# Optimization experiments

Measured on AMD Instinct MI355X. Metric: run time of the kernel, lower is better.

The kernel has to match this reference:

```python
import jax, jax.numpy as jnp
import numpy as np

N_NODES = 50000
N_EDGES = 300000
IN_DIM = 2000
DF = 128
H1, H2, OUT_DIM, K = 256, 128, 32, 4


def gcn_conv(x, W, b, src, dst, ew):
    """PyG GCNConv with edge weights: add self-loops (weight 1), symmetric norm."""
    N = x.shape[0]
    loop = jnp.arange(N)
    src2 = jnp.concatenate([src, loop])
    dst2 = jnp.concatenate([dst, loop])
    ew2 = jnp.concatenate([ew, jnp.ones((N,), ew.dtype)])
    deg = jax.ops.segment_sum(ew2, dst2, num_segments=N)
    dinv = jnp.where(deg > 0, jax.lax.rsqrt(deg), 0.0)
    norm = dinv[src2] * ew2 * dinv[dst2]            # [E+N]
    h = x @ W                                       # [N, out]
    out = jax.ops.segment_sum(norm[:, None] * h[src2], dst2, num_segments=N)
    return out + b


def setup_inputs() -> dict:
    key = jax.random.key(0)
    ks = jax.random.split(key, 13)
    p = lambda k, shape, s=0.05: (jax.random.normal(k, shape, jnp.float32) * s)
    return {
        "X": jax.random.normal(ks[0], (N_NODES, IN_DIM), jnp.float32),
        "edge_index": jax.random.randint(ks[1], (2, N_EDGES), 0, N_NODES),
        "Wh": p(ks[2], (IN_DIM, DF)),
        "mlp_W1": p(ks[3], (K, 2 * DF, 2)),
        "mlp_b1": jnp.zeros((K, 2), jnp.float32),
        "mlp_W2": p(ks[4], (K, 2, 1)),
        "mlp_b2": jnp.zeros((K, 1), jnp.float32),
        "g1_W": p(ks[5], (DF, H1)),
        "g1_b": jnp.zeros((H1,), jnp.float32),
        "g2_W": p(ks[6], (H1, H2)),
        "g2_b": jnp.zeros((H2,), jnp.float32),
        "fc_W": p(ks[7], (H2, OUT_DIM)),
        "fc_b": jnp.zeros((OUT_DIM,), jnp.float32),
    }


def reference(X, edge_index, Wh, mlp_W1, mlp_b1, mlp_W2, mlp_b2,
              g1_W, g1_b, g2_W, g2_b, fc_W, fc_b):
    src, dst = edge_index[0], edge_index[1]
    h0 = X @ Wh                                          # [N, df]
    edge_h = jnp.concatenate([h0[src], h0[dst]], axis=1)  # [E, 2df]
    # all K per-edge MLPs at once: hidden dim is just 2
    hid = jax.nn.relu(jnp.einsum('ef,kfh->keh', edge_h, mlp_W1) + mlp_b1[:, None, :])
    Gk = jax.nn.sigmoid(jnp.einsum('keh,kho->keo', hid, mlp_W2) + mlp_b2[:, None, :])[..., 0]  # [K, E]

    def autoencoder(ew):
        z1 = jax.nn.relu(gcn_conv(h0, g1_W, g1_b, src, dst, ew))
        z2 = jax.nn.relu(gcn_conv(z1, g2_W, g2_b, src, dst, ew))
        return jnp.mean(z2, axis=0) @ fc_W + fc_b         # [out_dim]

    descriptors = jax.vmap(autoencoder)(Gk)               # [K, out_dim]
    return descriptors, Gk
```

## Files before the change

### kernel.cpp

```cpp
#include <hip/hip_runtime.h>

#define NN 50000
#define NE 300000
#define INDIM 2000
#define KPAD 2048

typedef float f32x4 __attribute__((ext_vector_type(4)));
typedef __bf16 bf16x8 __attribute__((ext_vector_type(8)));
typedef unsigned short u16x8 __attribute__((ext_vector_type(8)));
typedef unsigned int u32;
typedef __attribute__((address_space(3))) u32 lds_u32;
typedef const __attribute__((address_space(1))) u32 glb_u32;

__device__ __forceinline__ unsigned short f2bf(float f) {
  return __builtin_bit_cast(unsigned short, (__bf16)f);
}
__device__ __forceinline__ float bf2f(unsigned short h) {
  union { unsigned u; float f; } v; v.u = ((unsigned)h) << 16;
  return v.f;
}

__global__ __launch_bounds__(256) void prep_kernel(
    const float* __restrict__ Wh, const float* __restrict__ g1,
    const float* __restrict__ g2, const float* __restrict__ W1,
    unsigned short* __restrict__ WhT, unsigned short* __restrict__ g1T,
    unsigned short* __restrict__ g2T, float* __restrict__ Wc)
{
  int i = blockIdx.x * 256 + threadIdx.x;
  if (i < 128 * KPAD) {
    int n = i >> 11, k = i & (KPAD - 1);
    WhT[i] = (k < INDIM) ? f2bf(Wh[(size_t)k * 128 + n]) : (unsigned short)0;
    return;
  }
  i -= 128 * KPAD;
  if (i < 256 * 128) {
    int n = i >> 7, k = i & 127;
    g1T[i] = f2bf(g1[(size_t)k * 256 + n]);
    return;
  }
  i -= 256 * 128;
  if (i < 128 * 256) {
    int n = i >> 8, k = i & 255;
    g2T[i] = f2bf(g2[(size_t)k * 128 + n]);
    return;
  }
  i -= 128 * 256;
  if (i < 2048) {
    int f = i >> 4, o = i & 15;
    int k = (o & 7) >> 1, h = o & 1;
    int fr = (o < 8) ? f : (128 + f);
    Wc[i] = W1[(size_t)k * 512 + fr * 2 + h];
  }
}

template<int A_F32>
__global__ __launch_bounds__(256) void gemm_kernel(
    const void* __restrict__ Aptr, const unsigned short* __restrict__ BT,
    unsigned short* __restrict__ C, int M, int N, int Ka, int Kb, int nkb)
{
  __shared__ unsigned short Alds[128 * 64];
  __shared__ unsigned short Blds[128 * 64];
  const int tid = threadIdx.x, lane = tid & 63, wv = tid >> 6;
  const int mBase = blockIdx.x * 128, nBase = blockIdx.y * 128;
  const int wrow = (wv >> 1) * 64, wcol = (wv & 1) * 64;
  const int lr = lane >> 3, lk8 = (lane & 7) * 8;
  const int swzCol = (((lane & 7) ^ lr) << 3);
  const int stIdx = lr * 64 + swzCol;
  f32x4 acc[4][4] = {};

  for (int kb = 0; kb < nkb; ++kb) {
    int k0 = kb * 64;
    #pragma unroll
    for (int i = 0; i < 4; ++i) {
      int chunk = wv * 4 + i;
      int brow = nBase + chunk * 8 + lr;
      __builtin_amdgcn_global_load_lds(
          (glb_u32*)(BT + (size_t)brow * Kb + k0 + swzCol),
          (lds_u32*)&Blds[chunk * 512 + lane * 8], 16, 0, 0);
    }
    if (A_F32) {
      const float* Af = (const float*)Aptr;
      #pragma unroll
      for (int i = 0; i < 4; ++i) {
        int chunk = wv * 4 + i;
        int rg = mBase + chunk * 8 + lr; if (rg > M - 1) rg = M - 1;
        int kc = k0 + lk8; if (kc > Ka - 8) kc = Ka - 8;
        const float4* s = (const float4*)(Af + (size_t)rg * Ka + kc);
        float4 f0 = s[0], f1 = s[1];
        u16x8 v;
        v[0]=f2bf(f0.x); v[1]=f2bf(f0.y); v[2]=f2bf(f0.z); v[3]=f2bf(f0.w);
        v[4]=f2bf(f1.x); v[5]=f2bf(f1.y); v[6]=f2bf(f1.z); v[7]=f2bf(f1.w);
        *(u16x8*)&Alds[chunk * 512 + stIdx] = v;
      }
    } else {
      const unsigned short* Ab = (const unsigned short*)Aptr;
      #pragma unroll
      for (int i = 0; i < 4; ++i) {
        int chunk = wv * 4 + i;
        int rg = mBase + chunk * 8 + lr; if (rg > M - 1) rg = M - 1;
        __builtin_amdgcn_global_load_lds(
            (glb_u32*)(Ab + (size_t)rg * Ka + k0 + swzCol),
            (lds_u32*)&Alds[chunk * 512 + lane * 8], 16, 0, 0);
      }
    }
    __syncthreads();
    #pragma unroll
    for (int kk = 0; kk < 2; ++kk) {
      const int r16 = lane & 15;
      const int slot = kk * 4 + (lane >> 4);
      bf16x8 a[4], b[4];
      #pragma unroll
      for (int mf = 0; mf < 4; ++mf) {
        int row = wrow + mf * 16 + r16;
        a[mf] = __builtin_bit_cast(bf16x8,
            *(const u16x8*)&Alds[row * 64 + ((slot ^ (row & 7)) << 3)]);
      }
      #pragma unroll
      for (int nf = 0; nf < 4; ++nf) {
        int row = wcol + nf * 16 + r16;
        b[nf] = __builtin_bit_cast(bf16x8,
            *(const u16x8*)&Blds[row * 64 + ((slot ^ (row & 7)) << 3)]);
      }
      #pragma unroll
      for (int mf = 0; mf < 4; ++mf)
        #pragma unroll
        for (int nf = 0; nf < 4; ++nf)
          acc[mf][nf] = __builtin_amdgcn_mfma_f32_16x16x32_bf16(a[mf], b[nf], acc[mf][nf], 0, 0, 0);
    }
    __syncthreads();
  }

  const int r16 = lane & 15, r4 = (lane >> 4) * 4;
  #pragma unroll
  for (int mf = 0; mf < 4; ++mf) {
    #pragma unroll
    for (int j = 0; j < 4; ++j) {
      int row = mBase + wrow + mf * 16 + r4 + j;
      if (row < M) {
        #pragma unroll
        for (int nf = 0; nf < 4; ++nf) {
          int col = nBase + wcol + nf * 16 + r16;
          C[(size_t)row * N + col] = f2bf(acc[mf][nf][j]);
        }
      }
    }
  }
}

__global__ __launch_bounds__(256) void p_kernel(const unsigned short* __restrict__ h0,
    const float* __restrict__ Wc, float* __restrict__ P)
{
  __shared__ float wl[2048];
  for (int i = threadIdx.x; i < 2048; i += 256) wl[i] = Wc[i];
  __syncthreads();
  int n = blockIdx.x * 256 + threadIdx.x;
  if (n >= NN) return;
  const unsigned short* hr = h0 + (size_t)n * 128;
  float acc[16];
  #pragma unroll
  for (int o = 0; o < 16; ++o) acc[o] = 0.f;
  for (int f8 = 0; f8 < 128; f8 += 8) {
    u16x8 hv = *(const u16x8*)(hr + f8);
    #pragma unroll
    for (int j = 0; j < 8; ++j) {
      float v = bf2f(hv[j]);
      #pragma unroll
      for (int o = 0; o < 16; ++o) acc[o] += v * wl[(f8 + j) * 16 + o];
    }
  }
  #pragma unroll
  for (int o = 0; o < 16; ++o) P[(size_t)n * 16 + o] = acc[o];
}

__global__ __launch_bounds__(256) void init_kernel(float* deg, int* hist, float* colsum)
{
  int i = blockIdx.x * 256 + threadIdx.x;
  if (i < 4 * NN) deg[i] = 1.0f;
  if (i < NN) hist[i] = 0;
  if (i < 512) colsum[i] = 0.f;
}

__global__ __launch_bounds__(256) void gk_kernel(
    const int* __restrict__ ei, const float* __restrict__ P,
    const float* __restrict__ b1, const float* __restrict__ W2,
    const float* __restrict__ b2, float* __restrict__ GkOut,
    float4* __restrict__ Gk4, float* __restrict__ deg, int* __restrict__ hist)
{
  int e = blockIdx.x * 256 + threadIdx.x;
  if (e >= NE) return;
  int s = ei[e], d = ei[NE + e];
  const float4* Ps = (const float4*)(P + (size_t)s * 16);
  const float4* Pd = (const float4*)(P + (size_t)d * 16);
  float4 p1a = Ps[0], p1b = Ps[1];
  float4 p2a = Pd[2], p2b = Pd[3];
  float p1[8] = {p1a.x, p1a.y, p1a.z, p1a.w, p1b.x, p1b.y, p1b.z, p1b.w};
  float p2[8] = {p2a.x, p2a.y, p2a.z, p2a.w, p2b.x, p2b.y, p2b.z, p2b.w};
  float g[4];
  #pragma unroll
  for (int k = 0; k < 4; ++k) {
    float h0v = p1[2*k]   + p2[2*k]   + b1[2*k];
    float h1v = p1[2*k+1] + p2[2*k+1] + b1[2*k+1];
    h0v = h0v > 0.f ? h0v : 0.f;
    h1v = h1v > 0.f ? h1v : 0.f;
    float pre = h0v * W2[2*k] + h1v * W2[2*k+1] + b2[k];
    g[k] = 1.f / (1.f + expf(-pre));
    GkOut[(size_t)k * NE + e] = g[k];
    atomicAdd(&deg[(size_t)d * 4 + k], g[k]);
  }
  Gk4[e] = make_float4(g[0], g[1], g[2], g[3]);
  atomicAdd(&hist[d], 1);
}

__global__ __launch_bounds__(256) void scan1_kernel(const int* __restrict__ hist,
    int* __restrict__ excl, int* __restrict__ bsum)
{
  __shared__ int sm[256];
  int t = threadIdx.x, i = blockIdx.x * 256 + t;
  int v = (i < NN) ? hist[i] : 0;
  sm[t] = v;
  __syncthreads();
  for (int off = 1; off < 256; off <<= 1) {
    int y = (t >= off) ? sm[t - off] : 0;
    __syncthreads();
    sm[t] += y;
    __syncthreads();
  }
  if (i < NN) excl[i] = sm[t] - v;
  if (t == 255) bsum[blockIdx.x] = sm[255];
}

__global__ __launch_bounds__(256) void scan2_kernel(int* bsum, int nb)
{
  __shared__ int sm[256];
  int t = threadIdx.x;
  int v = (t < nb) ? bsum[t] : 0;
  sm[t] = v;
  __syncthreads();
  for (int off = 1; off < 256; off <<= 1) {
    int y = (t >= off) ? sm[t - off] : 0;
    __syncthreads();
    sm[t] += y;
    __syncthreads();
  }
  if (t < nb) bsum[t] = sm[t] - v;
}

__global__ __launch_bounds__(256) void scan3_kernel(int* __restrict__ rowstart,
    const int* __restrict__ bsum, int* __restrict__ cursor)
{
  int i = blockIdx.x * 256 + threadIdx.x;
  if (i < NN) {
    int v = rowstart[i] + bsum[blockIdx.x];
    rowstart[i] = v;
    cursor[i] = v;
  }
  if (i == 0) rowstart[NN] = NE;
}

__global__ __launch_bounds__(256) void dinv_kernel(const float* __restrict__ deg,
    float* __restrict__ dinv)
{
  int i = blockIdx.x * 256 + threadIdx.x;
  if (i < 4 * NN) dinv[i] = rsqrtf(deg[i]);
}

__global__ __launch_bounds__(256) void csr_kernel(const int* __restrict__ ei,
    int* __restrict__ cursor, int* __restrict__ csr_s, int* __restrict__ csr_e)
{
  int e = blockIdx.x * 256 + threadIdx.x;
  if (e >= NE) return;
  int s = ei[e], d = ei[NE + e];
  int pos = atomicAdd(&cursor[d], 1);
  csr_s[pos] = s;
  csr_e[pos] = e;
}

__global__ __launch_bounds__(256) void csrw_kernel(const int* __restrict__ csr_s,
    const int* __restrict__ csr_e, const float4* __restrict__ Gk4,
    const float4* __restrict__ dinv4, float4* __restrict__ w4)
{
  int p = blockIdx.x * 256 + threadIdx.x;
  if (p >= NE) return;
  int s = csr_s[p], e = csr_e[p];
  float4 g = Gk4[e];
  float4 dv = dinv4[s];
  float4 w;
  w.x = g.x * dv.x;
  w.y = g.y * dv.y;
  w.z = g.z * dv.z;
  w.w = g.w * dv.w;
  w4[p] = w;
}

__global__ __launch_bounds__(256) void aggA_kernel(
    const unsigned short* __restrict__ H1, unsigned short* __restrict__ Z1,
    const float4* __restrict__ dinv4, const int* __restrict__ rowstart,
    const int* __restrict__ csr_s, const float4* __restrict__ w4,
    const float* __restrict__ g1b)
{
  const int lane = threadIdx.x & 63;
  const int wv = threadIdx.x >> 6;
  const int gw = blockIdx.x * 4 + wv;
  const int nw = gridDim.x * 4;
  const int c0 = lane * 4;
  float bb[4];
  #pragma unroll
  for (int c = 0; c < 4; ++c) bb[c] = g1b[c0 + c];
  for (int n = gw; n < NN; n += nw) {
    float4 dv = dinv4[n];
    float dd[4] = { dv.x, dv.y, dv.z, dv.w };
    uint2 sv = *(const uint2*)(H1 + (size_t)n * 256 + c0);
    float sf[4] = { bf2f((unsigned short)(sv.x & 0xFFFF)), bf2f((unsigned short)(sv.x >> 16)),
                    bf2f((unsigned short)(sv.y & 0xFFFF)), bf2f((unsigned short)(sv.y >> 16)) };
    float acc[4][4];
    #pragma unroll
    for (int k = 0; k < 4; ++k)
      #pragma unroll
      for (int c = 0; c < 4; ++c) acc[k][c] = dd[k] * sf[c];
    int rs = rowstart[n], re = rowstart[n + 1];
    for (int p = rs; p < re; ++p) {
      int s = csr_s[p];
      float4 w = w4[p];
      uint2 hv = *(const uint2*)(H1 + (size_t)s * 256 + c0);
      float hf[4] = { bf2f((unsigned short)(hv.x & 0xFFFF)), bf2f((unsigned short)(hv.x >> 16)),
                      bf2f((unsigned short)(hv.y & 0xFFFF)), bf2f((unsigned short)(hv.y >> 16)) };
      #pragma unroll
      for (int c = 0; c < 4; ++c) {
        acc[0][c] += w.x * hf[c];
        acc[1][c] += w.y * hf[c];
        acc[2][c] += w.z * hf[c];
        acc[3][c] += w.w * hf[c];
      }
    }
    #pragma unroll
    for (int k = 0; k < 4; ++k) {
      uint2 ov;
      float z0 = dd[k] * acc[k][0] + bb[0]; z0 = z0 > 0.f ? z0 : 0.f;
      float z1 = dd[k] * acc[k][1] + bb[1]; z1 = z1 > 0.f ? z1 : 0.f;
      float z2 = dd[k] * acc[k][2] + bb[2]; z2 = z2 > 0.f ? z2 : 0.f;
      float z3 = dd[k] * acc[k][3] + bb[3]; z3 = z3 > 0.f ? z3 : 0.f;
      ov.x = (unsigned)f2bf(z0) | ((unsigned)f2bf(z1) << 16);
      ov.y = (unsigned)f2bf(z2) | ((unsigned)f2bf(z3) << 16);
      *(uint2*)(Z1 + ((size_t)n * 4 + k) * 256 + c0) = ov;
    }
  }
}

__global__ __launch_bounds__(256) void aggB_kernel(
    const unsigned short* __restrict__ Y2, const float4* __restrict__ dinv4,
    const int* __restrict__ rowstart, const int* __restrict__ csr_s,
    const float4* __restrict__ w4, const float* __restrict__ g2b,
    float* __restrict__ colsum)
{
  const int lane = threadIdx.x & 63;
  const int wv = threadIdx.x >> 6;
  const int gw = blockIdx.x * 4 + wv;
  const int nw = gridDim.x * 4;
  const int kk = lane >> 4;
  const int c0 = (lane & 15) * 8;
  float bb[8];
  #pragma unroll
  for (int j = 0; j < 8; ++j) bb[j] = g2b[c0 + j];
  float s[8] = {};
  for (int n = gw; n < NN; n += nw) {
    float4 dv = dinv4[n];
    float dd = kk == 0 ? dv.x : kk == 1 ? dv.y : kk == 2 ? dv.z : dv.w;
    u16x8 sv = *(const u16x8*)(Y2 + (size_t)n * 512 + lane * 8);
    float a[8];
    #pragma unroll
    for (int j = 0; j < 8; ++j) a[j] = dd * bf2f(sv[j]);
    int rs = rowstart[n], re = rowstart[n + 1];
    for (int p = rs; p < re; ++p) {
      int src = csr_s[p];
      float4 w4v = w4[p];
      float w = kk == 0 ? w4v.x : kk == 1 ? w4v.y : kk == 2 ? w4v.z : w4v.w;
      u16x8 hv = *(const u16x8*)(Y2 + (size_t)src * 512 + lane * 8);
      #pragma unroll
      for (int j = 0; j < 8; ++j) a[j] += w * bf2f(hv[j]);
    }
    #pragma unroll
    for (int j = 0; j < 8; ++j) {
      float z = dd * a[j] + bb[j];
      s[j] += z > 0.f ? z : 0.f;
    }
  }
  __shared__ float lsum[4 * 512];
  #pragma unroll
  for (int j = 0; j < 8; ++j) lsum[wv * 512 + kk * 128 + c0 + j] = s[j];
  __syncthreads();
  for (int i = threadIdx.x; i < 512; i += 256)
    atomicAdd(&colsum[i], lsum[i] + lsum[512 + i] + lsum[1024 + i] + lsum[1536 + i]);
}

__global__ void desc_kernel(const float* __restrict__ colsum,
    const float* __restrict__ fcW, const float* __restrict__ fcb,
    float* __restrict__ out)
{
  int t = threadIdx.x;
  if (t >= 128) return;
  int k = t >> 5, o = t & 31;
  float acc = 0.f;
  for (int c = 0; c < 128; ++c)
    acc += colsum[k * 128 + c] * fcW[c * 32 + o];
  out[t] = acc * (1.f / (float)NN) + fcb[o];
}

extern "C" void kernel_launch(void* const* d_in, const int* in_sizes, int n_in,
                              void* d_out, int out_size, void* d_ws, size_t ws_size,
                              hipStream_t stream)
{
  (void)in_sizes; (void)n_in; (void)out_size; (void)ws_size;
  const float* X   = (const float*)d_in[0];
  const int*   ei  = (const int*)d_in[1];
  const float* Wh  = (const float*)d_in[2];
  const float* W1  = (const float*)d_in[3];
  const float* b1  = (const float*)d_in[4];
  const float* W2  = (const float*)d_in[5];
  const float* b2  = (const float*)d_in[6];
  const float* g1W = (const float*)d_in[7];
  const float* g1b = (const float*)d_in[8];
  const float* g2W = (const float*)d_in[9];
  const float* g2b = (const float*)d_in[10];
  const float* fcW = (const float*)d_in[11];
  const float* fcb = (const float*)d_in[12];
  float* out = (float*)d_out;

  char* ws = (char*)d_ws;
  size_t off = 0;
  auto alloc = [&](size_t bytes) -> void* {
    void* p = ws + off; off += (bytes + 255) & ~(size_t)255; return p;
  };
  unsigned short* WhT = (unsigned short*)alloc((size_t)128 * KPAD * 2);
  unsigned short* g1T = (unsigned short*)alloc((size_t)256 * 128 * 2);
  unsigned short* g2T = (unsigned short*)alloc((size_t)128 * 256 * 2);
  float* Wc  = (float*)alloc(2048 * 4);
  unsigned short* h0 = (unsigned short*)alloc((size_t)NN * 128 * 2);
  unsigned short* H1 = (unsigned short*)alloc((size_t)NN * 256 * 2);
  float* P   = (float*)alloc((size_t)NN * 16 * 4);
  float* deg = (float*)alloc((size_t)4 * NN * 4);
  float* dinv= (float*)alloc((size_t)4 * NN * 4);
  int* hist  = (int*)alloc((size_t)NN * 4);
  int* rowst = (int*)alloc((size_t)(NN + 1) * 4);
  int* cursor= (int*)alloc((size_t)NN * 4);
  int* bsum  = (int*)alloc(256 * 4);
  int* csr_s = (int*)alloc((size_t)NE * 4);
  int* csr_e = (int*)alloc((size_t)NE * 4);
  float4* Gk4 = (float4*)alloc((size_t)NE * 16);
  float4* w4  = (float4*)alloc((size_t)NE * 16);
  unsigned short* Z1 = (unsigned short*)alloc((size_t)4 * NN * 256 * 2);
  unsigned short* Y2 = (unsigned short*)alloc((size_t)4 * NN * 128 * 2);
  float* colsum = (float*)alloc(512 * 4);

  float* GkOut = out + 128;
  const int gEdge = (NE + 255) / 256;

  prep_kernel<<<(128*KPAD + 256*128 + 128*256 + 2048 + 255)/256, 256, 0, stream>>>(
      Wh, g1W, g2W, W1, WhT, g1T, g2T, Wc);
  init_kernel<<<(4*NN + 255)/256, 256, 0, stream>>>(deg, hist, colsum);
  gemm_kernel<1><<<dim3(391, 1), 256, 0, stream>>>(
      X, WhT, h0, NN, 128, INDIM, KPAD, KPAD / 64);
  gemm_kernel<0><<<dim3(391, 2), 256, 0, stream>>>(
      h0, g1T, H1, NN, 256, 128, 128, 2);
  p_kernel<<<196, 256, 0, stream>>>(h0, Wc, P);
  gk_kernel<<<gEdge, 256, 0, stream>>>(ei, P, b1, W2, b2, GkOut, Gk4, deg, hist);
  scan1_kernel<<<196, 256, 0, stream>>>(hist, rowst, bsum);
  scan2_kernel<<<1, 256, 0, stream>>>(bsum, 196);
  scan3_kernel<<<196, 256, 0, stream>>>(rowst, bsum, cursor);
  dinv_kernel<<<(4*NN + 255)/256, 256, 0, stream>>>(deg, dinv);
  csr_kernel<<<gEdge, 256, 0, stream>>>(ei, cursor, csr_s, csr_e);
  csrw_kernel<<<gEdge, 256, 0, stream>>>(csr_s, csr_e, Gk4, (const float4*)dinv, w4);
  aggA_kernel<<<2048, 256, 0, stream>>>(H1, Z1, (const float4*)dinv, rowst, csr_s, w4, g1b);
  gemm_kernel<0><<<dim3(1563, 1), 256, 0, stream>>>(
      Z1, g2T, Y2, 4 * NN, 128, 256, 256, 4);
  aggB_kernel<<<2048, 256, 0, stream>>>(
      Y2, (const float4*)dinv, rowst, csr_s, w4, g2b, colsum);
  desc_kernel<<<1, 128, 0, stream>>>(colsum, fcW, fcb, out);
}
```

Measured before the change: 891.5 us.

## Fuse init, dinv and CSR weight kernels; prefetch next edge in aggregation loops

Folds init into prep_kernel, dinv computation into scan3, and csrw into csr_kernel, which drops the csr_e array and three launches. The aggregation loops in aggA and aggB now load the next edge's source, weight and feature row before accumulating the current one, a software-pipelining step meant to hide gather latency. The trade-off is more registers per thread in the aggregation kernels and scattered w4 writes from the CSR kernel.

Result: faster. 873.4 us (-2.0%).

```diff
diff --git a/kernel.cpp b/kernel.cpp
--- a/kernel.cpp
+++ b/kernel.cpp
@@ -24,7 +24,8 @@
     const float* __restrict__ Wh, const float* __restrict__ g1,
     const float* __restrict__ g2, const float* __restrict__ W1,
     unsigned short* __restrict__ WhT, unsigned short* __restrict__ g1T,
-    unsigned short* __restrict__ g2T, float* __restrict__ Wc)
+    unsigned short* __restrict__ g2T, float* __restrict__ Wc,
+    float* __restrict__ deg, int* __restrict__ hist, float* __restrict__ colsum)
 {
   int i = blockIdx.x * 256 + threadIdx.x;
   if (i < 128 * KPAD) {
@@ -50,6 +51,13 @@
     int k = (o & 7) >> 1, h = o & 1;
     int fr = (o < 8) ? f : (128 + f);
     Wc[i] = W1[(size_t)k * 512 + fr * 2 + h];
+    return;
+  }
+  i -= 2048;
+  if (i < 4 * NN) {
+    deg[i] = 1.0f;
+    if (i < NN) hist[i] = 0;
+    if (i < 512) colsum[i] = 0.f;
   }
 }
 
@@ -172,14 +180,6 @@
   for (int o = 0; o < 16; ++o) P[(size_t)n * 16 + o] = acc[o];
 }
 
-__global__ __launch_bounds__(256) void init_kernel(float* deg, int* hist, float* colsum)
-{
-  int i = blockIdx.x * 256 + threadIdx.x;
-  if (i < 4 * NN) deg[i] = 1.0f;
-  if (i < NN) hist[i] = 0;
-  if (i < 512) colsum[i] = 0.f;
-}
-
 __global__ __launch_bounds__(256) void gk_kernel(
     const int* __restrict__ ei, const float* __restrict__ P,
     const float* __restrict__ b1, const float* __restrict__ W2,
@@ -246,42 +246,33 @@
 }
 
 __global__ __launch_bounds__(256) void scan3_kernel(int* __restrict__ rowstart,
-    const int* __restrict__ bsum, int* __restrict__ cursor)
+    const int* __restrict__ bsum, int* __restrict__ cursor,
+    const float4* __restrict__ deg4, float4* __restrict__ dinv4)
 {
   int i = blockIdx.x * 256 + threadIdx.x;
   if (i < NN) {
     int v = rowstart[i] + bsum[blockIdx.x];
     rowstart[i] = v;
     cursor[i] = v;
+    float4 dg = deg4[i];
+    float4 dv;
+    dv.x = rsqrtf(dg.x); dv.y = rsqrtf(dg.y);
+    dv.z = rsqrtf(dg.z); dv.w = rsqrtf(dg.w);
+    dinv4[i] = dv;
   }
   if (i == 0) rowstart[NN] = NE;
 }
 
-__global__ __launch_bounds__(256) void dinv_kernel(const float* __restrict__ deg,
-    float* __restrict__ dinv)
-{
-  int i = blockIdx.x * 256 + threadIdx.x;
-  if (i < 4 * NN) dinv[i] = rsqrtf(deg[i]);
-}
-
 __global__ __launch_bounds__(256) void csr_kernel(const int* __restrict__ ei,
-    int* __restrict__ cursor, int* __restrict__ csr_s, int* __restrict__ csr_e)
+    int* __restrict__ cursor, const float4* __restrict__ Gk4,
+    const float4* __restrict__ dinv4, int* __restrict__ csr_s,
+    float4* __restrict__ w4)
 {
   int e = blockIdx.x * 256 + threadIdx.x;
   if (e >= NE) return;
   int s = ei[e], d = ei[NE + e];
   int pos = atomicAdd(&cursor[d], 1);
   csr_s[pos] = s;
-  csr_e[pos] = e;
-}
-
-__global__ __launch_bounds__(256) void csrw_kernel(const int* __restrict__ csr_s,
-    const int* __restrict__ csr_e, const float4* __restrict__ Gk4,
-    const float4* __restrict__ dinv4, float4* __restrict__ w4)
-{
-  int p = blockIdx.x * 256 + threadIdx.x;
-  if (p >= NE) return;
-  int s = csr_s[p], e = csr_e[p];
   float4 g = Gk4[e];
   float4 dv = dinv4[s];
   float4 w;
@@ -289,7 +280,7 @@
   w.y = g.y * dv.y;
   w.z = g.z * dv.z;
   w.w = g.w * dv.w;
-  w4[p] = w;
+  w4[pos] = w;
 }
 
 __global__ __launch_bounds__(256) void aggA_kernel(
@@ -318,18 +309,33 @@
       #pragma unroll
       for (int c = 0; c < 4; ++c) acc[k][c] = dd[k] * sf[c];
     int rs = rowstart[n], re = rowstart[n + 1];
-    for (int p = rs; p < re; ++p) {
-      int s = csr_s[p];
-      float4 w = w4[p];
-      uint2 hv = *(const uint2*)(H1 + (size_t)s * 256 + c0);
-      float hf[4] = { bf2f((unsigned short)(hv.x & 0xFFFF)), bf2f((unsigned short)(hv.x >> 16)),
-                      bf2f((unsigned short)(hv.y & 0xFFFF)), bf2f((unsigned short)(hv.y >> 16)) };
+    if (rs < re) {
+      int sC = csr_s[rs];
+      float4 wC = w4[rs];
+      uint2 hC = *(const uint2*)(H1 + (size_t)sC * 256 + c0);
+      for (int p = rs + 1; p < re; ++p) {
+        int sNx = csr_s[p];
+        float4 wN = w4[p];
+        uint2 hN = *(const uint2*)(H1 + (size_t)sNx * 256 + c0);
+        float hf[4] = { bf2f((unsigned short)(hC.x & 0xFFFF)), bf2f((unsigned short)(hC.x >> 16)),
+                        bf2f((unsigned short)(hC.y & 0xFFFF)), bf2f((unsigned short)(hC.y >> 16)) };
+        #pragma unroll
+        for (int c = 0; c < 4; ++c) {
+          acc[0][c] += wC.x * hf[c];
+          acc[1][c] += wC.y * hf[c];
+          acc[2][c] += wC.z * hf[c];
+          acc[3][c] += wC.w * hf[c];
+        }
+        wC = wN; hC = hN;
+      }
+      float hf[4] = { bf2f((unsigned short)(hC.x & 0xFFFF)), bf2f((unsigned short)(hC.x >> 16)),
+                      bf2f((unsigned short)(hC.y & 0xFFFF)), bf2f((unsigned short)(hC.y >> 16)) };
       #pragma unroll
       for (int c = 0; c < 4; ++c) {
-        acc[0][c] += w.x * hf[c];
-        acc[1][c] += w.y * hf[c];
-        acc[2][c] += w.z * hf[c];
-        acc[3][c] += w.w * hf[c];
+        acc[0][c] += wC.x * hf[c];
+        acc[1][c] += wC.y * hf[c];
+        acc[2][c] += wC.z * hf[c];
+        acc[3][c] += wC.w * hf[c];
       }
     }
     #pragma unroll
@@ -370,13 +376,22 @@
     #pragma unroll
     for (int j = 0; j < 8; ++j) a[j] = dd * bf2f(sv[j]);
     int rs = rowstart[n], re = rowstart[n + 1];
-    for (int p = rs; p < re; ++p) {
-      int src = csr_s[p];
-      float4 w4v = w4[p];
-      float w = kk == 0 ? w4v.x : kk == 1 ? w4v.y : kk == 2 ? w4v.z : w4v.w;
-      u16x8 hv = *(const u16x8*)(Y2 + (size_t)src * 512 + lane * 8);
-      #pragma unroll
-      for (int j = 0; j < 8; ++j) a[j] += w * bf2f(hv[j]);
+    if (rs < re) {
+      int sC = csr_s[rs];
+      float4 wC4 = w4[rs];
+      u16x8 hC = *(const u16x8*)(Y2 + (size_t)sC * 512 + lane * 8);
+      for (int p = rs + 1; p < re; ++p) {
+        int sNx = csr_s[p];
+        float4 wN4 = w4[p];
+        u16x8 hN = *(const u16x8*)(Y2 + (size_t)sNx * 512 + lane * 8);
+        float w = kk == 0 ? wC4.x : kk == 1 ? wC4.y : kk == 2 ? wC4.z : wC4.w;
+        #pragma unroll
+        for (int j = 0; j < 8; ++j) a[j] += w * bf2f(hC[j]);
+        wC4 = wN4; hC = hN;
+      }
+      float w = kk == 0 ? wC4.x : kk == 1 ? wC4.y : kk == 2 ? wC4.z : wC4.w;
+      #pragma unroll
+      for (int j = 0; j < 8; ++j) a[j] += w * bf2f(hC[j]);
     }
     #pragma unroll
     for (int j = 0; j < 8; ++j) {
@@ -444,7 +459,6 @@
   int* cursor= (int*)alloc((size_t)NN * 4);
   int* bsum  = (int*)alloc(256 * 4);
   int* csr_s = (int*)alloc((size_t)NE * 4);
-  int* csr_e = (int*)alloc((size_t)NE * 4);
   float4* Gk4 = (float4*)alloc((size_t)NE * 16);
   float4* w4  = (float4*)alloc((size_t)NE * 16);
   unsigned short* Z1 = (unsigned short*)alloc((size_t)4 * NN * 256 * 2);
@@ -453,10 +467,10 @@
 
   float* GkOut = out + 128;
   const int gEdge = (NE + 255) / 256;
-
-  prep_kernel<<<(128*KPAD + 256*128 + 128*256 + 2048 + 255)/256, 256, 0, stream>>>(
-      Wh, g1W, g2W, W1, WhT, g1T, g2T, Wc);
-  init_kernel<<<(4*NN + 255)/256, 256, 0, stream>>>(deg, hist, colsum);
+  const int gPrep = (128*KPAD + 256*128 + 128*256 + 2048 + 4*NN + 255) / 256;
+
+  prep_kernel<<<gPrep, 256, 0, stream>>>(
+      Wh, g1W, g2W, W1, WhT, g1T, g2T, Wc, deg, hist, colsum);
   gemm_kernel<1><<<dim3(391, 1), 256, 0, stream>>>(
       X, WhT, h0, NN, 128, INDIM, KPAD, KPAD / 64);
   gemm_kernel<0><<<dim3(391, 2), 256, 0, stream>>>(
@@ -465,10 +479,10 @@
   gk_kernel<<<gEdge, 256, 0, stream>>>(ei, P, b1, W2, b2, GkOut, Gk4, deg, hist);
   scan1_kernel<<<196, 256, 0, stream>>>(hist, rowst, bsum);
   scan2_kernel<<<1, 256, 0, stream>>>(bsum, 196);
-  scan3_kernel<<<196, 256, 0, stream>>>(rowst, bsum, cursor);
-  dinv_kernel<<<(4*NN + 255)/256, 256, 0, stream>>>(deg, dinv);
-  csr_kernel<<<gEdge, 256, 0, stream>>>(ei, cursor, csr_s, csr_e);
-  csrw_kernel<<<gEdge, 256, 0, stream>>>(csr_s, csr_e, Gk4, (const float4*)dinv, w4);
+  scan3_kernel<<<196, 256, 0, stream>>>(rowst, bsum, cursor,
+      (const float4*)deg, (float4*)dinv);
+  csr_kernel<<<gEdge, 256, 0, stream>>>(ei, cursor, Gk4, (const float4*)dinv,
+      csr_s, w4);
   aggA_kernel<<<2048, 256, 0, stream>>>(H1, Z1, (const float4*)dinv, rowst, csr_s, w4, g1b);
   gemm_kernel<0><<<dim3(1563, 1), 256, 0, stream>>>(
       Z1, g2T, Y2, 4 * NN, 128, 256, 256, 4);
```
